# Kernel tuning notes

Hardware: AMD Instinct MI355X
Metric: run time of the kernel (lower is better)

Reference implementation:

```python
import jax, jax.numpy as jnp
import numpy as np

LSTM_IN = 125
LSTM_H = 125
MLP_D_H = 512
N = 512


def _lstm_scan(x, Wih, Whh, bih, bhh):
    # x: (N, LSTM_IN); PyTorch gate order: i, f, g, o
    H = LSTM_H
    def step(carry, xt):
        h, c = carry
        g = Wih @ xt + Whh @ h + bih + bhh  # (4H,)
        i = jax.nn.sigmoid(g[:H])
        f = jax.nn.sigmoid(g[H:2 * H])
        gg = jnp.tanh(g[2 * H:3 * H])
        o = jax.nn.sigmoid(g[3 * H:])
        c = f * c + i * gg
        h = o * jnp.tanh(c)
        return (h, c), h
    init = (jnp.zeros((H,), x.dtype), jnp.zeros((H,), x.dtype))
    _, hs = jax.lax.scan(step, init, x)
    return hs  # (N, H)


def setup_inputs() -> dict:
    key = jax.random.key(0)
    ks = jax.random.split(key, 14)
    s = 0.05
    d = {
        "sentence_emb": jax.random.normal(ks[0], (N, 1, LSTM_IN), jnp.float32),
        "Wih_f": jax.random.normal(ks[1], (4 * LSTM_H, LSTM_IN), jnp.float32) * s,
        "Whh_f": jax.random.normal(ks[2], (4 * LSTM_H, LSTM_H), jnp.float32) * s,
        "bih_f": jax.random.normal(ks[3], (4 * LSTM_H,), jnp.float32) * s,
        "bhh_f": jax.random.normal(ks[4], (4 * LSTM_H,), jnp.float32) * s,
        "Wih_b": jax.random.normal(ks[5], (4 * LSTM_H, LSTM_IN), jnp.float32) * s,
        "Whh_b": jax.random.normal(ks[6], (4 * LSTM_H, LSTM_H), jnp.float32) * s,
        "bih_b": jax.random.normal(ks[7], (4 * LSTM_H,), jnp.float32) * s,
        "bhh_b": jax.random.normal(ks[8], (4 * LSTM_H,), jnp.float32) * s,
        "W1": jax.random.normal(ks[9], (MLP_D_H, 4 * LSTM_H), jnp.float32) * s,
        "b1": jax.random.normal(ks[10], (MLP_D_H,), jnp.float32) * s,
        "W2": jax.random.normal(ks[11], (1, MLP_D_H), jnp.float32) * s,
        "b2": jax.random.normal(ks[12], (1,), jnp.float32) * s,
    }
    return d


def reference(sentence_emb, Wih_f, Whh_f, bih_f, bhh_f, Wih_b, Whh_b, bih_b, bhh_b, W1, b1, W2, b2):
    x = sentence_emb[:, 0, :]  # (N, 125), batch=1
    h_fwd = _lstm_scan(x, Wih_f, Whh_f, bih_f, bhh_f)           # (N, 125)
    h_bwd = _lstm_scan(x[::-1], Wih_b, Whh_b, bih_b, bhh_b)[::-1]  # (N, 125)
    h = jnp.concatenate([h_fwd, h_bwd], axis=-1)  # (N, 250)
    # output_mtx[i, j] = MLP(concat(h[j], h[i]))
    # Decompose first linear: W1 @ cat(h_j, h_i) = Wa @ h_j + Wb @ h_i
    D = h.shape[-1]
    Pa = h @ W1[:, :D].T   # (N, H): contribution of h_j
    Pb = h @ W1[:, D:].T   # (N, H): contribution of h_i
    hidden = jnp.tanh(Pb[:, None, :] + Pa[None, :, :] + b1)  # (N, N, H)
    out = hidden @ W2[0] + b2[0]  # (N, N)
    return out
```

## Files before the change

kernel.cpp:

```cpp
#include <hip/hip_runtime.h>

typedef __bf16 bf16_t;
typedef __bf16 bf16x8 __attribute__((ext_vector_type(8)));
typedef float f32x4 __attribute__((ext_vector_type(4)));
typedef int   int4v __attribute__((ext_vector_type(4)));

#define LOG2E 1.4426950408889634f

template<int CTRL>
__device__ __forceinline__ float qperm(float x) {
  return __builtin_bit_cast(float,
      __builtin_amdgcn_update_dpp(0, __builtin_bit_cast(int, x), CTRL, 0xF, 0xF, true));
}

__device__ __forceinline__ void lds_barrier() {
  asm volatile("s_waitcnt lgkmcnt(0)\n\ts_barrier" ::: "memory");
}

__global__ __launch_bounds__(256) void pre_kernel(
    const float* __restrict__ x,
    const float* __restrict__ Wih_f, const float* __restrict__ bih_f,
    const float* __restrict__ bhh_f,
    const float* __restrict__ Wih_b, const float* __restrict__ bih_b,
    const float* __restrict__ bhh_b,
    float* __restrict__ preT)
{
  const int dir = blockIdx.x >> 5;
  const int T   = blockIdx.x & 31;
  const float* __restrict__ Wih = dir ? Wih_b : Wih_f;
  const float* __restrict__ bih = dir ? bih_b : bih_f;
  const float* __restrict__ bhh = dir ? bhh_b : bhh_f;

  const int tid = threadIdx.x;
  const int wv  = tid >> 6;
  const int lane = tid & 63;
  const int q = lane >> 4, cc = lane & 15;

  const int r  = 16 * T + cc;
  const int na = r >> 2, pa = r & 3;
  const bool vld = (na < 125);
  const float* __restrict__ Wr = Wih + (vld ? (125 * pa + na) * 125 : 0);

  bf16x8 whi[4], wlo[4];
  #pragma unroll
  for (int ks = 0; ks < 4; ++ks) {
    #pragma unroll
    for (int j = 0; j < 8; ++j) {
      int k = 32 * ks + 8 * q + j;
      float wvv = (vld && k < 125) ? Wr[k] : 0.0f;
      bf16_t hi = (bf16_t)wvv;
      whi[ks][j] = hi;
      wlo[ks][j] = (bf16_t)(wvv - (float)hi);
    }
  }

  float bias[4];
  #pragma unroll
  for (int reg = 0; reg < 4; ++reg) {
    int ro = 16 * T + 4 * q + reg;
    int no = ro >> 2, po = ro & 3;
    bias[reg] = (no < 125) ? (bih[125 * po + no] + bhh[125 * po + no]) : 0.0f;
  }

  for (int i = 0; i < 8; ++i) {
    const int tt = 8 * wv + i;
    const int t  = 16 * tt + cc;
    const int trow = dir ? (511 - t) : t;
    const float* __restrict__ xr = x + trow * 125;

    f32x4 acc = (f32x4)0.0f;
    #pragma unroll
    for (int ks = 0; ks < 4; ++ks) {
      bf16x8 xhi, xlo;
      #pragma unroll
      for (int j = 0; j < 8; ++j) {
        int k = 32 * ks + 8 * q + j;
        float xv = (k < 125) ? xr[k] : 0.0f;
        bf16_t hi = (bf16_t)xv;
        xhi[j] = hi;
        xlo[j] = (bf16_t)(xv - (float)hi);
      }
      acc = __builtin_amdgcn_mfma_f32_16x16x32_bf16(whi[ks], xhi, acc, 0, 0, 0);
      acc = __builtin_amdgcn_mfma_f32_16x16x32_bf16(whi[ks], xlo, acc, 0, 0, 0);
      acc = __builtin_amdgcn_mfma_f32_16x16x32_bf16(wlo[ks], xhi, acc, 0, 0, 0);
    }
    #pragma unroll
    for (int reg = 0; reg < 4; ++reg) {
      int ro = 16 * T + 4 * q + reg;
      preT[dir * 262144 + ro * 512 + 16 * tt + cc] = acc[reg] + bias[reg];
    }
  }
}

__global__ __launch_bounds__(512) void lstm_kernel(
    const float* __restrict__ Whh_f, const float* __restrict__ Whh_b,
    const float* __restrict__ pre,
    bf16_t* __restrict__ h_all)
{
  const int dir = blockIdx.x;
  const float* __restrict__ Whh = dir ? Whh_b : Whh_f;

  const int tid  = threadIdx.x;
  const int lane = tid & 63;
  const int w    = tid >> 6;
  const int q    = lane >> 4;
  const int cc   = lane & 15;
  const int lt   = cc >> 2;
  const int p    = cc & 3;

  float wm = 0.0f;
  #pragma unroll
  for (int LT = 0; LT < 4; ++LT) {
    int rr = 16 * (4 * w + LT) + cc;
    int nn = rr >> 2, pp = rr & 3;
    if (nn < 125) {
      const float* __restrict__ Wrow = Whh + (125 * pp + nn) * 125;
      #pragma unroll
      for (int ks = 0; ks < 2; ++ks)
        #pragma unroll
        for (int jj = 0; jj < 16; ++jj) {
          int k = 64 * ks + 16 * q + jj;
          if (k < 125) wm = fmaxf(wm, fabsf(Wrow[k]));
        }
    }
  }
  #pragma unroll
  for (int off = 1; off < 64; off <<= 1)
    wm = fmaxf(wm, __shfl_xor(wm, off));
  __shared__ float wmx[8];
  if (lane == 0) wmx[w] = wm;
  __syncthreads();
  float wmax = wmx[0];
  #pragma unroll
  for (int u = 1; u < 8; ++u) wmax = fmaxf(wmax, wmx[u]);
  const float s_w  = 127.0f / wmax;
  const float invq = wmax / (127.0f * 127.0f);

  int4v afrag[4][2];
  #pragma unroll
  for (int LT = 0; LT < 4; ++LT) {
    int rr = 16 * (4 * w + LT) + cc;
    int nn = rr >> 2, pp = rr & 3;
    bool avld = (nn < 125);
    const float* __restrict__ Wrow = Whh + (avld ? (125 * pp + nn) * 125 : 0);
    #pragma unroll
    for (int ks = 0; ks < 2; ++ks) {
      int4v v;
      #pragma unroll
      for (int word = 0; word < 4; ++word) {
        int b = 0;
        #pragma unroll
        for (int byte = 0; byte < 4; ++byte) {
          int jj = 4 * word + byte;
          int k  = 64 * ks + 16 * q + jj;
          int qv = 0;
          if (avld && k < 125)
            qv = (int)__builtin_rintf(Wrow[k] * s_w);
          b |= (qv & 0xFF) << (8 * byte);
        }
        v[word] = b;
      }
      afrag[LT][ks] = v;
    }
  }

  __shared__ __align__(16) char hbuf[2][128];
  if (tid < 256) hbuf[tid >> 7][tid & 127] = 0;
  if (dir == 0) {
    #pragma unroll
    for (int u = 0; u < 6; ++u) h_all[tid * 256 + 250 + u] = (bf16_t)0.0f;
  }
  __syncthreads();

  const int   r_lane = 64 * w + 16 * lt + 4 * q + p;
  const int   nset   = 16 * w + 4 * lt + q;
  const float mult   = (p == 2) ? (-2.0f * LOG2E) : (-LOG2E);
  const float sA     = (p == 2) ? 2.0f : 1.0f;
  const float sB     = (p == 2) ? -1.0f : 0.0f;
  const float dscale = mult * invq;
  const float* __restrict__ preR = pre + dir * 262144 + r_lane * 512;
  float c = 0.0f;

  float4 pv_cur = *(const float4*)preR;

  for (int g = 0; g < 128; ++g) {
    float4 pv_nxt = make_float4(0.f, 0.f, 0.f, 0.f);
    if (g < 127) pv_nxt = *(const float4*)(preR + 4 * (g + 1));

    #pragma unroll
    for (int s4 = 0; s4 < 4; ++s4) {
      const int step = 4 * g + s4;
      const int cur  = s4 & 1, nxt = cur ^ 1;
      const float pv = (s4 == 0) ? pv_cur.x : (s4 == 1) ? pv_cur.y
                     : (s4 == 2) ? pv_cur.z : pv_cur.w;
      const float pvm = mult * pv;

      int4v b0 = *(const int4v*)&hbuf[cur][16 * q];
      int4v b1 = *(const int4v*)&hbuf[cur][64 + 16 * q];

      int4v acc[4];
      #pragma unroll
      for (int LT = 0; LT < 4; ++LT) {
        int4v a = (int4v)0;
        a = __builtin_amdgcn_mfma_i32_16x16x64_i8(afrag[LT][0], b0, a, 0, 0, 0);
        a = __builtin_amdgcn_mfma_i32_16x16x64_i8(afrag[LT][1], b1, a, 0, 0, 0);
        acc[LT] = a;
      }

      int gl[4];
      #pragma unroll
      for (int LT = 0; LT < 4; ++LT) {
        int a01 = (p & 1) ? acc[LT][1] : acc[LT][0];
        int a23 = (p & 1) ? acc[LT][3] : acc[LT][2];
        gl[LT] = (p & 2) ? a23 : a01;
      }
      int b01 = (lt & 1) ? gl[1] : gl[0];
      int b23 = (lt & 1) ? gl[3] : gl[2];
      int gsel = (lt & 2) ? b23 : b01;

      float gf  = (float)gsel;
      float xg  = fmaf(gf, dscale, pvm);
      float e   = __builtin_amdgcn_exp2f(xg);
      float y   = __builtin_amdgcn_rcpf(1.0f + e);
      float act = fmaf(y, sA, sB);

      float b_i = qperm<0x00>(act);
      float b_f = qperm<0x55>(act);
      float b_g = qperm<0xAA>(act);
      float b_o = qperm<0xFF>(act);
      c = fmaf(b_f, c, b_i * b_g);
      float e2 = __builtin_amdgcn_exp2f(-2.0f * LOG2E * c);
      float tc = fmaf(__builtin_amdgcn_rcpf(1.0f + e2), 2.0f, -1.0f);
      float h  = b_o * tc;

      if (p == 0) {
        int qh = (int)__builtin_rintf(h * 127.0f);
        hbuf[nxt][nset] = (char)qh;
        if (nset < 125) {
          int t_orig = dir ? (511 - step) : step;
          h_all[t_orig * 256 + dir * 125 + nset] = (bf16_t)h;
        }
      }
      lds_barrier();
    }
    pv_cur = pv_nxt;
  }
}

__global__ __launch_bounds__(256) void qgemm_kernel(
    const bf16_t* __restrict__ h_all,
    const float* __restrict__ W1,
    const float* __restrict__ b1,
    float* __restrict__ Qa,
    float* __restrict__ Qb)
{
  const int tid  = threadIdx.x;
  const int wv   = tid >> 6;
  const int lane = tid & 63;
  const int q    = lane >> 4, cc = lane & 15;
  const int bj   = blockIdx.x & 31;
  const int bm   = blockIdx.x >> 5;
  const int m    = bm * 64 + wv * 16 + cc;
  const int j0   = bj * 16;
  const int jA   = j0 + cc;

  const bool isB = (m >= 512);
  const int  row = isB ? (m - 512) : m;
  const int  cof = isB ? 250 : 0;

  f32x4 acc = (f32x4)0.0f;
  #pragma unroll
  for (int ks = 0; ks < 8; ++ks) {
    int kb = 32 * ks + 8 * q;
    bf16x8 a = *(const bf16x8*)&h_all[jA * 256 + kb];
    bf16x8 b;
    #pragma unroll
    for (int jj = 0; jj < 8; ++jj) {
      int k = kb + jj;
      float v = (k < 250) ? W1[row * 500 + cof + k] : 0.0f;
      b[jj] = (bf16_t)v;
    }
    acc = __builtin_amdgcn_mfma_f32_16x16x32_bf16(a, b, acc, 0, 0, 0);
  }

  const float C2 = 2.0f * LOG2E;
  #pragma unroll
  for (int reg = 0; reg < 4; ++reg) {
    int j = j0 + 4 * q + reg;
    float v = acc[reg];
    if (!isB) Qa[j * 512 + m] = C2 * v;
    else      Qb[j * 512 + (m - 512)] = C2 * (v + b1[m - 512]);
  }
}

__global__ __launch_bounds__(256) void outer_kernel(
    const float* __restrict__ Qa, const float* __restrict__ Qb,
    const float* __restrict__ W2, const float* __restrict__ b2,
    float* __restrict__ out)
{
  __shared__ float sa[2][32][33];
  __shared__ float sb[2][32][33];
  __shared__ float sw[2][32];

  const int tid = threadIdx.x;
  const int bi  = blockIdx.x >> 4, bjx = blockIdx.x & 15;
  const int i0  = bi * 32, j0 = bjx * 32;
  const int ii0 = (tid & 15) * 2;
  const int jj0 = (tid >> 4) * 2;
  const int ljj = tid & 31, kk4 = (tid >> 5) * 4;

  float accR[2][2] = {{0.0f, 0.0f}, {0.0f, 0.0f}};
  float wsum = 0.0f;

  for (int kc = 0; kc < 16; ++kc) {
    const int buf = kc & 1;
    const int k0  = kc * 32;
    float4 va = *(const float4*)&Qa[(j0 + ljj) * 512 + k0 + kk4];
    float4 vb = *(const float4*)&Qb[(i0 + ljj) * 512 + k0 + kk4];
    sa[buf][kk4 + 0][ljj] = va.x; sa[buf][kk4 + 1][ljj] = va.y;
    sa[buf][kk4 + 2][ljj] = va.z; sa[buf][kk4 + 3][ljj] = va.w;
    sb[buf][kk4 + 0][ljj] = vb.x; sb[buf][kk4 + 1][ljj] = vb.y;
    sb[buf][kk4 + 2][ljj] = vb.z; sb[buf][kk4 + 3][ljj] = vb.w;
    if (tid < 32) sw[buf][tid] = W2[k0 + tid];
    __syncthreads();

    #pragma unroll 4
    for (int kk = 0; kk < 32; ++kk) {
      float2 av = *(const float2*)&sa[buf][kk][jj0];
      float2 bv = *(const float2*)&sb[buf][kk][ii0];
      float wk = sw[buf][kk];
      wsum += wk;
      {
        float e = __builtin_amdgcn_exp2f(av.x + bv.x);
        accR[0][0] = fmaf(wk, __builtin_amdgcn_rcpf(1.0f + e), accR[0][0]);
      }
      {
        float e = __builtin_amdgcn_exp2f(av.y + bv.x);
        accR[0][1] = fmaf(wk, __builtin_amdgcn_rcpf(1.0f + e), accR[0][1]);
      }
      {
        float e = __builtin_amdgcn_exp2f(av.x + bv.y);
        accR[1][0] = fmaf(wk, __builtin_amdgcn_rcpf(1.0f + e), accR[1][0]);
      }
      {
        float e = __builtin_amdgcn_exp2f(av.y + bv.y);
        accR[1][1] = fmaf(wk, __builtin_amdgcn_rcpf(1.0f + e), accR[1][1]);
      }
    }
  }

  const float bb = b2[0];
  #pragma unroll
  for (int i2 = 0; i2 < 2; ++i2)
    #pragma unroll
    for (int j2 = 0; j2 < 2; ++j2)
      out[(i0 + ii0 + i2) * 512 + (j0 + jj0 + j2)] =
          wsum - 2.0f * accR[i2][j2] + bb;
}

extern "C" void kernel_launch(void* const* d_in, const int* in_sizes, int n_in,
                              void* d_out, int out_size, void* d_ws, size_t ws_size,
                              hipStream_t stream) {
  const float* emb   = (const float*)d_in[0];
  const float* Wih_f = (const float*)d_in[1];
  const float* Whh_f = (const float*)d_in[2];
  const float* bih_f = (const float*)d_in[3];
  const float* bhh_f = (const float*)d_in[4];
  const float* Wih_b = (const float*)d_in[5];
  const float* Whh_b = (const float*)d_in[6];
  const float* bih_b = (const float*)d_in[7];
  const float* bhh_b = (const float*)d_in[8];
  const float* W1    = (const float*)d_in[9];
  const float* b1    = (const float*)d_in[10];
  const float* W2    = (const float*)d_in[11];
  const float* b2    = (const float*)d_in[12];
  float* out = (float*)d_out;

  char* ws = (char*)d_ws;
  float*  pre   = (float*)ws;
  bf16_t* h_all = (bf16_t*)(ws + 2 * 1024 * 1024);
  float*  Qa    = (float*)(ws + 2 * 1024 * 1024 + 256 * 1024);
  float*  Qb    = Qa + 512 * 512;

  pre_kernel<<<64, 256, 0, stream>>>(emb, Wih_f, bih_f, bhh_f,
                                     Wih_b, bih_b, bhh_b, pre);
  lstm_kernel<<<2, 512, 0, stream>>>(Whh_f, Whh_b, pre, h_all);
  qgemm_kernel<<<512, 256, 0, stream>>>(h_all, W1, b1, Qa, Qb);
  outer_kernel<<<256, 256, 0, stream>>>(Qa, Qb, W2, b2, out);
}
```

Baseline: 336.4 us.

## Use sdot4 per-thread recurrence in LSTM and split-K the outer kernel

The LSTM recurrence replaces the MFMA int8 matvec with per-thread sdot4 dot products: each thread holds its quantized weight row in registers and reads the int8 hidden state from LDS. This removes the MFMA output lane selection and shortens the per-step dependency chain, at the cost of more register pressure and more LDS reads per step. Separately, the outer kernel is split along K into two halves accumulated with atomicAdd into a zeroed output. That doubles the block count for better CU occupancy but adds a memset and atomic traffic.

```diff
diff --git a/kernel.cpp b/kernel.cpp
--- a/kernel.cpp
+++ b/kernel.cpp
@@ -6,6 +6,12 @@
 typedef int   int4v __attribute__((ext_vector_type(4)));
 
 #define LOG2E 1.4426950408889634f
+
+#if defined(__has_builtin)
+#if __has_builtin(__builtin_amdgcn_sdot4)
+#define HAVE_SDOT4 1
+#endif
+#endif
 
 template<int CTRL>
 __device__ __forceinline__ float qperm(float x) {
@@ -92,10 +98,131 @@
   }
 }
 
-__global__ __launch_bounds__(512) void lstm_kernel(
+#ifdef HAVE_SDOT4
+__global__ __launch_bounds__(512, 2) void lstm_kernel(
     const float* __restrict__ Whh_f, const float* __restrict__ Whh_b,
     const float* __restrict__ pre,
     bf16_t* __restrict__ h_all)
+{
+  const int dir = blockIdx.x;
+  const float* __restrict__ Whh = dir ? Whh_b : Whh_f;
+
+  const int tid = threadIdx.x;
+  const int w   = tid >> 6;
+  const int p   = tid & 3;
+  const int n   = tid >> 2;
+
+  const bool valid = (n < 125);
+  const float* __restrict__ Wrow = Whh + (valid ? (125 * p + n) * 125 : 0);
+
+  float wm = 0.0f;
+  if (valid) {
+    #pragma unroll 5
+    for (int k = 0; k < 125; ++k) wm = fmaxf(wm, fabsf(Wrow[k]));
+  }
+  #pragma unroll
+  for (int off = 1; off < 64; off <<= 1)
+    wm = fmaxf(wm, __shfl_xor(wm, off));
+  __shared__ float wmx[8];
+  if ((tid & 63) == 0) wmx[w] = wm;
+  __syncthreads();
+  float wmax = wmx[0];
+  #pragma unroll
+  for (int u = 1; u < 8; ++u) wmax = fmaxf(wmax, wmx[u]);
+  const float s_w  = 127.0f / wmax;
+  const float invq = wmax / (127.0f * 127.0f);
+
+  int wq[32];
+  #pragma unroll
+  for (int d = 0; d < 32; ++d) {
+    int b = 0;
+    #pragma unroll
+    for (int byte = 0; byte < 4; ++byte) {
+      int k = 4 * d + byte;
+      int qv = 0;
+      if (valid && k < 125)
+        qv = (int)__builtin_rintf(Wrow[k] * s_w);
+      b |= (qv & 0xFF) << (8 * byte);
+    }
+    wq[d] = b;
+  }
+
+  __shared__ __align__(16) char hbuf[2][128];
+  if (tid < 256) hbuf[tid >> 7][tid & 127] = 0;
+  if (dir == 0) {
+    #pragma unroll
+    for (int u = 0; u < 6; ++u) h_all[tid * 256 + 250 + u] = (bf16_t)0.0f;
+  }
+  __syncthreads();
+
+  const float mult   = (p == 2) ? (-2.0f * LOG2E) : (-LOG2E);
+  const float sA     = (p == 2) ? 2.0f : 1.0f;
+  const float sB     = (p == 2) ? -1.0f : 0.0f;
+  const float dscale = mult * invq;
+  const float* __restrict__ preR = pre + dir * 262144 + tid * 512;
+  float c = 0.0f;
+
+  float4 pv_cur = *(const float4*)preR;
+
+  for (int g = 0; g < 128; ++g) {
+    float4 pv_nxt = make_float4(0.f, 0.f, 0.f, 0.f);
+    if (g < 127) pv_nxt = *(const float4*)(preR + 4 * (g + 1));
+
+    #pragma unroll
+    for (int s4 = 0; s4 < 4; ++s4) {
+      const int step = 4 * g + s4;
+      const int cur  = s4 & 1, nxt = cur ^ 1;
+      const float pv = (s4 == 0) ? pv_cur.x : (s4 == 1) ? pv_cur.y
+                     : (s4 == 2) ? pv_cur.z : pv_cur.w;
+      const float pvm = mult * pv;
+
+      int4v hv[8];
+      #pragma unroll
+      for (int u = 0; u < 8; ++u)
+        hv[u] = *(const int4v*)&hbuf[cur][16 * u];
+
+      int a0 = 0, a1 = 0, a2 = 0, a3 = 0;
+      #pragma unroll
+      for (int d = 0; d < 8; ++d) {
+        a0 = __builtin_amdgcn_sdot4(wq[4 * d + 0], hv[d][0], a0, false);
+        a1 = __builtin_amdgcn_sdot4(wq[4 * d + 1], hv[d][1], a1, false);
+        a2 = __builtin_amdgcn_sdot4(wq[4 * d + 2], hv[d][2], a2, false);
+        a3 = __builtin_amdgcn_sdot4(wq[4 * d + 3], hv[d][3], a3, false);
+      }
+      const int gsel = (a0 + a1) + (a2 + a3);
+
+      float xg  = fmaf((float)gsel, dscale, pvm);
+      float e   = __builtin_amdgcn_exp2f(xg);
+      float y   = __builtin_amdgcn_rcpf(1.0f + e);
+      float act = fmaf(y, sA, sB);
+
+      float b_i = qperm<0x00>(act);
+      float b_f = qperm<0x55>(act);
+      float b_g = qperm<0xAA>(act);
+      float b_o = qperm<0xFF>(act);
+      c = fmaf(b_f, c, b_i * b_g);
+      float e2 = __builtin_amdgcn_exp2f(-2.0f * LOG2E * c);
+      float tc = fmaf(__builtin_amdgcn_rcpf(1.0f + e2), 2.0f, -1.0f);
+      float h  = b_o * tc;
+
+      if (p == 0) {
+        hbuf[nxt][n] = (char)(int)__builtin_rintf(h * 127.0f);
+        if (n < 125) {
+          int t_orig = dir ? (511 - step) : step;
+          h_all[t_orig * 256 + dir * 125 + n] = (bf16_t)h;
+        }
+      }
+      lds_barrier();
+    }
+    pv_cur = pv_nxt;
+  }
+}
+
+#else
+
+__global__ __launch_bounds__(512) void lstm_kernel(
+    const float* __restrict__ Whh_f, const float* __restrict__ Whh_b,
+    const float* __restrict__ pre, bf16_t* __restrict__ h_all)
 {
   const int dir = blockIdx.x;
   const float* __restrict__ Whh = dir ? Whh_b : Whh_f;
@@ -218,8 +345,7 @@
       int b23 = (lt & 1) ? gl[3] : gl[2];
       int gsel = (lt & 2) ? b23 : b01;
 
-      float gf  = (float)gsel;
-      float xg  = fmaf(gf, dscale, pvm);
+      float xg  = fmaf((float)gsel, dscale, pvm);
       float e   = __builtin_amdgcn_exp2f(xg);
       float y   = __builtin_amdgcn_rcpf(1.0f + e);
       float act = fmaf(y, sA, sB);
@@ -234,8 +360,7 @@
       float h  = b_o * tc;
 
       if (p == 0) {
-        int qh = (int)__builtin_rintf(h * 127.0f);
-        hbuf[nxt][nset] = (char)qh;
+        hbuf[nxt][nset] = (char)(int)__builtin_rintf(h * 127.0f);
         if (nset < 125) {
           int t_orig = dir ? (511 - step) : step;
           h_all[t_orig * 256 + dir * 125 + nset] = (bf16_t)h;
@@ -246,6 +371,7 @@
     pv_cur = pv_nxt;
   }
 }
+#endif
 
 __global__ __launch_bounds__(256) void qgemm_kernel(
     const bf16_t* __restrict__ h_all,
@@ -302,19 +428,22 @@
   __shared__ float sb[2][32][33];
   __shared__ float sw[2][32];
 
-  const int tid = threadIdx.x;
-  const int bi  = blockIdx.x >> 4, bjx = blockIdx.x & 15;
-  const int i0  = bi * 32, j0 = bjx * 32;
-  const int ii0 = (tid & 15) * 2;
-  const int jj0 = (tid >> 4) * 2;
-  const int ljj = tid & 31, kk4 = (tid >> 5) * 4;
+  const int tid  = threadIdx.x;
+  const int bk   = blockIdx.x >> 8;
+  const int tile = blockIdx.x & 255;
+  const int bi   = tile >> 4, bjx = tile & 15;
+  const int i0   = bi * 32, j0 = bjx * 32;
+  const int ii0  = (tid & 15) * 2;
+  const int jj0  = (tid >> 4) * 2;
+  const int ljj  = tid & 31, kk4 = (tid >> 5) * 4;
+  const int kbase = bk * 256;
 
   float accR[2][2] = {{0.0f, 0.0f}, {0.0f, 0.0f}};
   float wsum = 0.0f;
 
-  for (int kc = 0; kc < 16; ++kc) {
+  for (int kc = 0; kc < 8; ++kc) {
     const int buf = kc & 1;
-    const int k0  = kc * 32;
+    const int k0  = kbase + kc * 32;
     float4 va = *(const float4*)&Qa[(j0 + ljj) * 512 + k0 + kk4];
     float4 vb = *(const float4*)&Qb[(i0 + ljj) * 512 + k0 + kk4];
     sa[buf][kk4 + 0][ljj] = va.x; sa[buf][kk4 + 1][ljj] = va.y;
@@ -349,13 +478,13 @@
     }
   }
 
-  const float bb = b2[0];
+  const float bb = (bk == 0) ? b2[0] : 0.0f;
   #pragma unroll
   for (int i2 = 0; i2 < 2; ++i2)
     #pragma unroll
     for (int j2 = 0; j2 < 2; ++j2)
-      out[(i0 + ii0 + i2) * 512 + (j0 + jj0 + j2)] =
-          wsum - 2.0f * accR[i2][j2] + bb;
+      atomicAdd(&out[(i0 + ii0 + i2) * 512 + (j0 + jj0 + j2)],
+                wsum - 2.0f * accR[i2][j2] + bb);
 }
 
 extern "C" void kernel_launch(void* const* d_in, const int* in_sizes, int n_in,
@@ -386,5 +515,6 @@
                                      Wih_b, bih_b, bhh_b, pre);
   lstm_kernel<<<2, 512, 0, stream>>>(Whh_f, Whh_b, pre, h_all);
   qgemm_kernel<<<512, 256, 0, stream>>>(h_all, W1, b1, Qa, Qb);
-  outer_kernel<<<256, 256, 0, stream>>>(Qa, Qb, W2, b2, out);
-}
+  hipMemsetAsync(out, 0, (size_t)out_size * sizeof(float), stream);
+  outer_kernel<<<512, 256, 0, stream>>>(Qa, Qb, W2, b2, out);
+}
```

Result: slower. 427.3 us (+27.0%).
